# Optimization experiments

Measured on AMD Instinct MI355X. Metric: run time of the kernel, lower is better.

## Reference

```python
import jax, jax.numpy as jnp
import numpy as np
from jax import lax

DT = 0.1
B, T, SD, CD, H = 1024, 200, 64, 32, 512


def setup_inputs() -> dict:
    key = jax.random.key(0)
    k0, k1, k2, k3 = jax.random.split(key, 4)
    scale1 = 1.0 / np.sqrt(SD + CD)
    scale2 = 1.0 / np.sqrt(H)
    return {
        "x0": jax.random.normal(k0, (B, SD), dtype=jnp.float32),
        "controls": jax.random.normal(k1, (B, T, CD), dtype=jnp.float32),
        "W1": jax.random.normal(k2, (SD + CD, H), dtype=jnp.float32) * scale1,
        "b1": jnp.zeros((H,), dtype=jnp.float32),
        "W2": jax.random.normal(k3, (H, SD), dtype=jnp.float32) * scale2,
        "b2": jnp.zeros((SD,), dtype=jnp.float32),
    }


def reference(x0, controls, W1, b1, W2, b2):
    # dynamics: x_{t+1} = x + dt * MLP(concat(x, u)); rollout with true data dependency
    def step(x, u):
        h = jnp.tanh(jnp.concatenate([x, u], axis=-1) @ W1 + b1)  # [B, H]
        x_next = x + DT * (h @ W2 + b2)                           # [B, SD]
        return x_next, x_next

    controls_t = jnp.swapaxes(controls, 0, 1)  # [T, B, CD]
    _, xs = lax.scan(step, x0, controls_t)     # xs: [T, B, SD]
    states = jnp.concatenate([x0[:, None, :], jnp.swapaxes(xs, 0, 1)], axis=1)  # [B, T+1, SD]
    return states
```

## Files before the change

### kernel.cpp

```cpp
#include <hip/hip_runtime.h>
#include <cstddef>


constexpr int B_  = 1024;
constexpr int T_  = 200;
constexpr int SD_ = 64;
constexpr int CD_ = 32;
constexpr int H_  = 512;
constexpr int KD_ = SD_ + CD_;
constexpr float DT_ = 0.1f;
constexpr int ROWS_ = 4;
constexpr int THREADS_ = 1024;
constexpr int KSLICES_ = 4;
constexpr int KLEN_ = KD_ / KSLICES_;
constexpr int CHUNK_ = 32;

typedef float f2 __attribute__((ext_vector_type(2)));

__global__ __launch_bounds__(THREADS_)
void rollout_r12_kernel(
    const float* __restrict__ x0,
    const float* __restrict__ ctrl,
    const float* __restrict__ W1,
    const float* __restrict__ b1,
    const float* __restrict__ W2,
    const float* __restrict__ b2,
    float* __restrict__ out)
{
    __shared__ float xcT[KD_][ROWS_];
    __shared__ float part1[KSLICES_][ROWS_][H_];
    __shared__ float pbuf[ROWS_][H_];
    __shared__ float part2[ROWS_][16][SD_];

    const int tid = threadIdx.x;
    const int r0  = blockIdx.x * ROWS_;

    const int jp    = tid & 255;
    const int ks    = tid >> 8;
    const int j0    = jp * 2;
    const int kbase = ks * KLEN_;
    f2 w1p[KLEN_];
    #pragma unroll
    for (int i = 0; i < KLEN_; ++i)
        w1p[i] = *(const f2*)&W1[(size_t)(kbase + i) * H_ + j0];

    const int wv = tid >> 6;
    const int sl = tid & 63;
    const int jb = wv * CHUNK_;
    float w2p[CHUNK_];
    #pragma unroll
    for (int i = 0; i < CHUNK_; ++i)
        w2p[i] = W2[(size_t)(jb + i) * SD_ + sl];

    const int rF  = tid >> 8;
    const int jjF = (tid & 255) * 2;
    const f2 bj2 = {b1[jjF], b1[jjF + 1]};

    const int rf = (tid >> 6) & 3;
    const int sf = tid & 63;
    const float bs = b2[sf];

    const int  lt = tid - 512;
    const bool loader = (lt >= 0) && (lt < ROWS_ * CD_);
    const int  lr = (lt >> 5) & 3;
    const int  lc = lt & 31;
    const size_t ctrl_base = (size_t)(r0 + lr) * T_ * CD_ + lc;

    if (tid < ROWS_ * SD_) {
        const float v = x0[(size_t)(r0 + rf) * SD_ + sf];
        xcT[sf][rf] = v;
        out[(size_t)(r0 + rf) * (T_ + 1) * SD_ + sf] = v;
    }
    if (loader) xcT[SD_ + lc][lr] = ctrl[ctrl_base];
    __syncthreads();

    for (int t = 0; t < T_; ++t) {
        float cpre = 0.f;
        if (loader && (t + 1 < T_))
            cpre = ctrl[ctrl_base + (size_t)(t + 1) * CD_];

        f2 a0 = {0.f, 0.f}, a1 = {0.f, 0.f}, a2 = {0.f, 0.f}, a3 = {0.f, 0.f};
        #pragma unroll
        for (int i = 0; i < KLEN_; ++i) {
            const float4 xv = *(const float4*)&xcT[kbase + i][0];
            const f2 w = w1p[i];
            a0 = __builtin_elementwise_fma(w, (f2){xv.x, xv.x}, a0);
            a1 = __builtin_elementwise_fma(w, (f2){xv.y, xv.y}, a1);
            a2 = __builtin_elementwise_fma(w, (f2){xv.z, xv.z}, a2);
            a3 = __builtin_elementwise_fma(w, (f2){xv.w, xv.w}, a3);
        }
        *(f2*)&part1[ks][0][j0] = a0;
        *(f2*)&part1[ks][1][j0] = a1;
        *(f2*)&part1[ks][2][j0] = a2;
        *(f2*)&part1[ks][3][j0] = a3;
        __syncthreads();

        {
            f2 s = *(const f2*)&part1[0][rF][jjF];
            s += *(const f2*)&part1[1][rF][jjF];
            s += *(const f2*)&part1[2][rF][jjF];
            s += *(const f2*)&part1[3][rF][jjF];
            s += bj2;
            f2 hv;
            hv.x = tanhf(s.x);
            hv.y = tanhf(s.y);
            *(f2*)&pbuf[rF][jjF] = hv;
            if (loader && (t + 1 < T_))
                xcT[SD_ + lc][lr] = cpre;
        }
        __syncthreads();

        {
            f2 q0 = {0.f, 0.f}, q1 = {0.f, 0.f}, q2 = {0.f, 0.f}, q3 = {0.f, 0.f};
            #pragma unroll
            for (int i4 = 0; i4 < CHUNK_; i4 += 4) {
                const f2 wab = {w2p[i4 + 0], w2p[i4 + 1]};
                const f2 wcd = {w2p[i4 + 2], w2p[i4 + 3]};
                const float4 h0 = *(const float4*)&pbuf[0][jb + i4];
                const float4 h1 = *(const float4*)&pbuf[1][jb + i4];
                const float4 h2 = *(const float4*)&pbuf[2][jb + i4];
                const float4 h3 = *(const float4*)&pbuf[3][jb + i4];
                q0 = __builtin_elementwise_fma((f2){h0.x, h0.y}, wab, q0);
                q0 = __builtin_elementwise_fma((f2){h0.z, h0.w}, wcd, q0);
                q1 = __builtin_elementwise_fma((f2){h1.x, h1.y}, wab, q1);
                q1 = __builtin_elementwise_fma((f2){h1.z, h1.w}, wcd, q1);
                q2 = __builtin_elementwise_fma((f2){h2.x, h2.y}, wab, q2);
                q2 = __builtin_elementwise_fma((f2){h2.z, h2.w}, wcd, q2);
                q3 = __builtin_elementwise_fma((f2){h3.x, h3.y}, wab, q3);
                q3 = __builtin_elementwise_fma((f2){h3.z, h3.w}, wcd, q3);
            }
            part2[0][wv][sl] = q0.x + q0.y;
            part2[1][wv][sl] = q1.x + q1.y;
            part2[2][wv][sl] = q2.x + q2.y;
            part2[3][wv][sl] = q3.x + q3.y;
        }
        __syncthreads();

        if (tid < ROWS_ * SD_) {
            float acc = part2[rf][0][sf];
            #pragma unroll
            for (int c = 1; c < 16; ++c) acc += part2[rf][c][sf];
            const float xnew = xcT[sf][rf] + DT_ * (acc + bs);
            xcT[sf][rf] = xnew;
            out[(size_t)(r0 + rf) * (T_ + 1) * SD_ + (size_t)(t + 1) * SD_ + sf] = xnew;
        }
        __syncthreads();
    }
}

extern "C" void kernel_launch(void* const* d_in, const int* in_sizes, int n_in,
                              void* d_out, int out_size, void* d_ws, size_t ws_size,
                              hipStream_t stream) {
    const float* x0   = (const float*)d_in[0];
    const float* ctrl = (const float*)d_in[1];
    const float* W1   = (const float*)d_in[2];
    const float* b1   = (const float*)d_in[3];
    const float* W2   = (const float*)d_in[4];
    const float* b2   = (const float*)d_in[5];
    float* out = (float*)d_out;

    dim3 grid(B_ / ROWS_);
    dim3 block(THREADS_);
    rollout_r12_kernel<<<grid, block, 0, stream>>>(x0, ctrl, W1, b1, W2, b2, out);
}
```

Before: 707.0 us.

## Reduce layer-1 K-slices with wave shuffles and stage W2 in shared memory

The four K-slices of the first matmul now sit in lanes of the same wavefront, so partial sums are combined with xor-shuffle butterflies instead of going through a shared-memory buffer. This removes one block-wide barrier per timestep. W2 moves from per-thread registers into a 128 KB shared array, which frees registers but adds LDS reads in the second matmul. b1 is also staged in shared memory, and the control-prefetch store moves after the barrier.

```diff
diff --git a/kernel.cpp b/kernel.cpp
--- a/kernel.cpp
+++ b/kernel.cpp
@@ -17,8 +17,17 @@
 
 typedef float f2 __attribute__((ext_vector_type(2)));
 
+__device__ __forceinline__ f2 bfly_ks(f2 v) {
+    f2 r;
+    r.x = __shfl_xor(v.x, 16);  r.y = __shfl_xor(v.y, 16);
+    v.x += r.x;                 v.y += r.y;
+    r.x = __shfl_xor(v.x, 32);  r.y = __shfl_xor(v.y, 32);
+    v.x += r.x;                 v.y += r.y;
+    return v;
+}
+
 __global__ __launch_bounds__(THREADS_)
-void rollout_r12_kernel(
+void rollout_r13_kernel(
     const float* __restrict__ x0,
     const float* __restrict__ ctrl,
     const float* __restrict__ W1,
@@ -27,34 +36,37 @@
     const float* __restrict__ b2,
     float* __restrict__ out)
 {
-    __shared__ float xcT[KD_][ROWS_];
-    __shared__ float part1[KSLICES_][ROWS_][H_];
-    __shared__ float pbuf[ROWS_][H_];
-    __shared__ float part2[ROWS_][16][SD_];
+    __shared__ __align__(16) float w2s[H_][SD_];
+    __shared__ __align__(16) float xcT[KD_][ROWS_];
+    __shared__ __align__(16) float pbuf[ROWS_][H_];
+    __shared__ __align__(16) float part2[ROWS_][16][SD_];
+    __shared__ __align__(16) float b1s[H_];
 
     const int tid = threadIdx.x;
     const int r0  = blockIdx.x * ROWS_;
 
-    const int jp    = tid & 255;
-    const int ks    = tid >> 8;
-    const int j0    = jp * 2;
+    const int lane = tid & 63;
+    const int wvid = tid >> 6;
+    const int ks   = lane >> 4;
+    const int jpl  = lane & 15;
+    const int j0   = (wvid * 16 + jpl) * 2;
     const int kbase = ks * KLEN_;
     f2 w1p[KLEN_];
     #pragma unroll
     for (int i = 0; i < KLEN_; ++i)
         w1p[i] = *(const f2*)&W1[(size_t)(kbase + i) * H_ + j0];
 
-    const int wv = tid >> 6;
-    const int sl = tid & 63;
-    const int jb = wv * CHUNK_;
-    float w2p[CHUNK_];
-    #pragma unroll
-    for (int i = 0; i < CHUNK_; ++i)
-        w2p[i] = W2[(size_t)(jb + i) * SD_ + sl];
+    {
+        const float4* __restrict__ src = (const float4*)W2;
+        float4* dst = (float4*)&w2s[0][0];
+        #pragma unroll
+        for (int i = 0; i < 8; ++i)
+            dst[i * THREADS_ + tid] = src[i * THREADS_ + tid];
+    }
+    if (tid < H_) b1s[tid] = b1[tid];
 
-    const int rF  = tid >> 8;
-    const int jjF = (tid & 255) * 2;
-    const f2 bj2 = {b1[jjF], b1[jjF + 1]};
+    const int sl = lane;
+    const int jb = wvid * CHUNK_;
 
     const int rf = (tid >> 6) & 3;
     const int sf = tid & 63;
@@ -89,33 +101,34 @@
             a2 = __builtin_elementwise_fma(w, (f2){xv.z, xv.z}, a2);
             a3 = __builtin_elementwise_fma(w, (f2){xv.w, xv.w}, a3);
         }
-        *(f2*)&part1[ks][0][j0] = a0;
-        *(f2*)&part1[ks][1][j0] = a1;
-        *(f2*)&part1[ks][2][j0] = a2;
-        *(f2*)&part1[ks][3][j0] = a3;
-        __syncthreads();
-
+        a0 = bfly_ks(a0);  a1 = bfly_ks(a1);
+        a2 = bfly_ks(a2);  a3 = bfly_ks(a3);
         {
-            f2 s = *(const f2*)&part1[0][rF][jjF];
-            s += *(const f2*)&part1[1][rF][jjF];
-            s += *(const f2*)&part1[2][rF][jjF];
-            s += *(const f2*)&part1[3][rF][jjF];
-            s += bj2;
+            const bool kb0 = (ks & 1) != 0;
+            const bool kb1 = (ks & 2) != 0;
+            const f2 s01 = kb0 ? a1 : a0;
+            const f2 s23 = kb0 ? a3 : a2;
+            const f2 sel = kb1 ? s23 : s01;
+            const f2 bj  = *(const f2*)&b1s[j0];
             f2 hv;
-            hv.x = tanhf(s.x);
-            hv.y = tanhf(s.y);
-            *(f2*)&pbuf[rF][jjF] = hv;
-            if (loader && (t + 1 < T_))
-                xcT[SD_ + lc][lr] = cpre;
+            hv.x = tanhf(sel.x + bj.x);
+            hv.y = tanhf(sel.y + bj.y);
+            *(f2*)&pbuf[ks][j0] = hv;
         }
         __syncthreads();
 
+        if (loader && (t + 1 < T_))
+            xcT[SD_ + lc][lr] = cpre;
         {
             f2 q0 = {0.f, 0.f}, q1 = {0.f, 0.f}, q2 = {0.f, 0.f}, q3 = {0.f, 0.f};
             #pragma unroll
             for (int i4 = 0; i4 < CHUNK_; i4 += 4) {
-                const f2 wab = {w2p[i4 + 0], w2p[i4 + 1]};
-                const f2 wcd = {w2p[i4 + 2], w2p[i4 + 3]};
+                const float wa = w2s[jb + i4 + 0][sl];
+                const float wb = w2s[jb + i4 + 1][sl];
+                const float wc = w2s[jb + i4 + 2][sl];
+                const float wd = w2s[jb + i4 + 3][sl];
+                const f2 wab = {wa, wb};
+                const f2 wcd = {wc, wd};
                 const float4 h0 = *(const float4*)&pbuf[0][jb + i4];
                 const float4 h1 = *(const float4*)&pbuf[1][jb + i4];
                 const float4 h2 = *(const float4*)&pbuf[2][jb + i4];
@@ -129,10 +142,10 @@
                 q3 = __builtin_elementwise_fma((f2){h3.x, h3.y}, wab, q3);
                 q3 = __builtin_elementwise_fma((f2){h3.z, h3.w}, wcd, q3);
             }
-            part2[0][wv][sl] = q0.x + q0.y;
-            part2[1][wv][sl] = q1.x + q1.y;
-            part2[2][wv][sl] = q2.x + q2.y;
-            part2[3][wv][sl] = q3.x + q3.y;
+            part2[0][wvid][sl] = q0.x + q0.y;
+            part2[1][wvid][sl] = q1.x + q1.y;
+            part2[2][wvid][sl] = q2.x + q2.y;
+            part2[3][wvid][sl] = q3.x + q3.y;
         }
         __syncthreads();
 
@@ -161,5 +174,5 @@
 
     dim3 grid(B_ / ROWS_);
     dim3 block(THREADS_);
-    rollout_r12_kernel<<<grid, block, 0, stream>>>(x0, ctrl, W1, b1, W2, b2, out);
+    rollout_r13_kernel<<<grid, block, 0, stream>>>(x0, ctrl, W1, b1, W2, b2, out);
 }
```

Result: slower. 827.8 us (+17.1%).

## Repartition both matmuls across threads with more K slices and paired outputs

Applied to the files above, without the earlier changes.

The first matmul moves from 4 to 8 K slices, and each thread now computes two column pairs 256 apart, so each LDS load of the shared input feeds twice as many FMAs. The second matmul switches to f2 outputs over paired state dims with 16-row h chunks, which doubles the number of partial sums to 32. The final reductions become trees to shorten dependency chains. The trade-off is more part1 and part2 LDS traffic and reduction work in exchange for fewer input loads per FMA, with unchanged register footprint.

```diff
diff --git a/kernel.cpp b/kernel.cpp
--- a/kernel.cpp
+++ b/kernel.cpp
@@ -11,14 +11,13 @@
 constexpr float DT_ = 0.1f;
 constexpr int ROWS_ = 4;
 constexpr int THREADS_ = 1024;
-constexpr int KSLICES_ = 4;
+constexpr int KSLICES_ = 8;
 constexpr int KLEN_ = KD_ / KSLICES_;
-constexpr int CHUNK_ = 32;
 
 typedef float f2 __attribute__((ext_vector_type(2)));
 
 __global__ __launch_bounds__(THREADS_)
-void rollout_r12_kernel(
+void rollout_r15_kernel(
     const float* __restrict__ x0,
     const float* __restrict__ ctrl,
     const float* __restrict__ W1,
@@ -27,30 +26,35 @@
     const float* __restrict__ b2,
     float* __restrict__ out)
 {
-    __shared__ float xcT[KD_][ROWS_];
-    __shared__ float part1[KSLICES_][ROWS_][H_];
-    __shared__ float pbuf[ROWS_][H_];
-    __shared__ float part2[ROWS_][16][SD_];
+    __shared__ __align__(16) float xcT[KD_][ROWS_];
+    __shared__ __align__(16) float part1[KSLICES_][ROWS_][H_];
+    __shared__ __align__(16) float pbuf[ROWS_][H_];
+    __shared__ __align__(16) float part2[ROWS_][32][SD_];
 
     const int tid = threadIdx.x;
     const int r0  = blockIdx.x * ROWS_;
 
-    const int jp    = tid & 255;
-    const int ks    = tid >> 8;
-    const int j0    = jp * 2;
+    const int jpg   = tid & 127;
+    const int ks    = tid >> 7;
+    const int j0    = jpg * 2;
     const int kbase = ks * KLEN_;
-    f2 w1p[KLEN_];
+    f2 w1a[KLEN_], w1b[KLEN_];
     #pragma unroll
-    for (int i = 0; i < KLEN_; ++i)
-        w1p[i] = *(const f2*)&W1[(size_t)(kbase + i) * H_ + j0];
+    for (int i = 0; i < KLEN_; ++i) {
+        w1a[i] = *(const f2*)&W1[(size_t)(kbase + i) * H_ + j0];
+        w1b[i] = *(const f2*)&W1[(size_t)(kbase + i) * H_ + j0 + 256];
+    }
 
-    const int wv = tid >> 6;
-    const int sl = tid & 63;
-    const int jb = wv * CHUNK_;
-    float w2p[CHUNK_];
+    const int wv    = tid >> 6;
+    const int lane  = tid & 63;
+    const int l5    = lane >> 5;
+    const int sfp   = lane & 31;
+    const int sf0   = sfp * 2;
+    const int hbase = wv * 32 + l5 * 16;
+    f2 w2p[16];
     #pragma unroll
-    for (int i = 0; i < CHUNK_; ++i)
-        w2p[i] = W2[(size_t)(jb + i) * SD_ + sl];
+    for (int i = 0; i < 16; ++i)
+        w2p[i] = *(const f2*)&W2[(size_t)(hbase + i) * SD_ + sf0];
 
     const int rF  = tid >> 8;
     const int jjF = (tid & 255) * 2;
@@ -79,28 +83,38 @@
         if (loader && (t + 1 < T_))
             cpre = ctrl[ctrl_base + (size_t)(t + 1) * CD_];
 
-        f2 a0 = {0.f, 0.f}, a1 = {0.f, 0.f}, a2 = {0.f, 0.f}, a3 = {0.f, 0.f};
+        f2 a0 = {0.f,0.f}, a1 = {0.f,0.f}, a2 = {0.f,0.f}, a3 = {0.f,0.f};
+        f2 b0 = {0.f,0.f}, b1v = {0.f,0.f}, b2v = {0.f,0.f}, b3 = {0.f,0.f};
         #pragma unroll
         for (int i = 0; i < KLEN_; ++i) {
             const float4 xv = *(const float4*)&xcT[kbase + i][0];
-            const f2 w = w1p[i];
-            a0 = __builtin_elementwise_fma(w, (f2){xv.x, xv.x}, a0);
-            a1 = __builtin_elementwise_fma(w, (f2){xv.y, xv.y}, a1);
-            a2 = __builtin_elementwise_fma(w, (f2){xv.z, xv.z}, a2);
-            a3 = __builtin_elementwise_fma(w, (f2){xv.w, xv.w}, a3);
+            const f2 wa = w1a[i];
+            const f2 wb = w1b[i];
+            a0  = __builtin_elementwise_fma(wa, (f2){xv.x, xv.x}, a0);
+            a1  = __builtin_elementwise_fma(wa, (f2){xv.y, xv.y}, a1);
+            a2  = __builtin_elementwise_fma(wa, (f2){xv.z, xv.z}, a2);
+            a3  = __builtin_elementwise_fma(wa, (f2){xv.w, xv.w}, a3);
+            b0  = __builtin_elementwise_fma(wb, (f2){xv.x, xv.x}, b0);
+            b1v = __builtin_elementwise_fma(wb, (f2){xv.y, xv.y}, b1v);
+            b2v = __builtin_elementwise_fma(wb, (f2){xv.z, xv.z}, b2v);
+            b3  = __builtin_elementwise_fma(wb, (f2){xv.w, xv.w}, b3);
         }
         *(f2*)&part1[ks][0][j0] = a0;
         *(f2*)&part1[ks][1][j0] = a1;
         *(f2*)&part1[ks][2][j0] = a2;
         *(f2*)&part1[ks][3][j0] = a3;
+        *(f2*)&part1[ks][0][j0 + 256] = b0;
+        *(f2*)&part1[ks][1][j0 + 256] = b1v;
+        *(f2*)&part1[ks][2][j0 + 256] = b2v;
+        *(f2*)&part1[ks][3][j0 + 256] = b3;
         __syncthreads();
 
         {
-            f2 s = *(const f2*)&part1[0][rF][jjF];
-            s += *(const f2*)&part1[1][rF][jjF];
-            s += *(const f2*)&part1[2][rF][jjF];
-            s += *(const f2*)&part1[3][rF][jjF];
-            s += bj2;
+            const f2 s0 = *(const f2*)&part1[0][rF][jjF] + *(const f2*)&part1[1][rF][jjF];
+            const f2 s1 = *(const f2*)&part1[2][rF][jjF] + *(const f2*)&part1[3][rF][jjF];
+            const f2 s2 = *(const f2*)&part1[4][rF][jjF] + *(const f2*)&part1[5][rF][jjF];
+            const f2 s3 = *(const f2*)&part1[6][rF][jjF] + *(const f2*)&part1[7][rF][jjF];
+            const f2 s  = ((s0 + s1) + (s2 + s3)) + bj2;
             f2 hv;
             hv.x = tanhf(s.x);
             hv.y = tanhf(s.y);
@@ -111,35 +125,48 @@
         __syncthreads();
 
         {
-            f2 q0 = {0.f, 0.f}, q1 = {0.f, 0.f}, q2 = {0.f, 0.f}, q3 = {0.f, 0.f};
+            f2 q0 = {0.f,0.f}, q1 = {0.f,0.f}, q2 = {0.f,0.f}, q3 = {0.f,0.f};
             #pragma unroll
-            for (int i4 = 0; i4 < CHUNK_; i4 += 4) {
-                const f2 wab = {w2p[i4 + 0], w2p[i4 + 1]};
-                const f2 wcd = {w2p[i4 + 2], w2p[i4 + 3]};
-                const float4 h0 = *(const float4*)&pbuf[0][jb + i4];
-                const float4 h1 = *(const float4*)&pbuf[1][jb + i4];
-                const float4 h2 = *(const float4*)&pbuf[2][jb + i4];
-                const float4 h3 = *(const float4*)&pbuf[3][jb + i4];
-                q0 = __builtin_elementwise_fma((f2){h0.x, h0.y}, wab, q0);
-                q0 = __builtin_elementwise_fma((f2){h0.z, h0.w}, wcd, q0);
-                q1 = __builtin_elementwise_fma((f2){h1.x, h1.y}, wab, q1);
-                q1 = __builtin_elementwise_fma((f2){h1.z, h1.w}, wcd, q1);
-                q2 = __builtin_elementwise_fma((f2){h2.x, h2.y}, wab, q2);
-                q2 = __builtin_elementwise_fma((f2){h2.z, h2.w}, wcd, q2);
-                q3 = __builtin_elementwise_fma((f2){h3.x, h3.y}, wab, q3);
-                q3 = __builtin_elementwise_fma((f2){h3.z, h3.w}, wcd, q3);
+            for (int i4 = 0; i4 < 16; i4 += 4) {
+                const float4 h0 = *(const float4*)&pbuf[0][hbase + i4];
+                const float4 h1 = *(const float4*)&pbuf[1][hbase + i4];
+                const float4 h2 = *(const float4*)&pbuf[2][hbase + i4];
+                const float4 h3 = *(const float4*)&pbuf[3][hbase + i4];
+                q0 = __builtin_elementwise_fma((f2){h0.x, h0.x}, w2p[i4 + 0], q0);
+                q0 = __builtin_elementwise_fma((f2){h0.y, h0.y}, w2p[i4 + 1], q0);
+                q0 = __builtin_elementwise_fma((f2){h0.z, h0.z}, w2p[i4 + 2], q0);
+                q0 = __builtin_elementwise_fma((f2){h0.w, h0.w}, w2p[i4 + 3], q0);
+                q1 = __builtin_elementwise_fma((f2){h1.x, h1.x}, w2p[i4 + 0], q1);
+                q1 = __builtin_elementwise_fma((f2){h1.y, h1.y}, w2p[i4 + 1], q1);
+                q1 = __builtin_elementwise_fma((f2){h1.z, h1.z}, w2p[i4 + 2], q1);
+                q1 = __builtin_elementwise_fma((f2){h1.w, h1.w}, w2p[i4 + 3], q1);
+                q2 = __builtin_elementwise_fma((f2){h2.x, h2.x}, w2p[i4 + 0], q2);
+                q2 = __builtin_elementwise_fma((f2){h2.y, h2.y}, w2p[i4 + 1], q2);
+                q2 = __builtin_elementwise_fma((f2){h2.z, h2.z}, w2p[i4 + 2], q2);
+                q2 = __builtin_elementwise_fma((f2){h2.w, h2.w}, w2p[i4 + 3], q2);
+                q3 = __builtin_elementwise_fma((f2){h3.x, h3.x}, w2p[i4 + 0], q3);
+                q3 = __builtin_elementwise_fma((f2){h3.y, h3.y}, w2p[i4 + 1], q3);
+                q3 = __builtin_elementwise_fma((f2){h3.z, h3.z}, w2p[i4 + 2], q3);
+                q3 = __builtin_elementwise_fma((f2){h3.w, h3.w}, w2p[i4 + 3], q3);
             }
-            part2[0][wv][sl] = q0.x + q0.y;
-            part2[1][wv][sl] = q1.x + q1.y;
-            part2[2][wv][sl] = q2.x + q2.y;
-            part2[3][wv][sl] = q3.x + q3.y;
+            const int c = wv * 2 + l5;
+            *(f2*)&part2[0][c][sf0] = q0;
+            *(f2*)&part2[1][c][sf0] = q1;
+            *(f2*)&part2[2][c][sf0] = q2;
+            *(f2*)&part2[3][c][sf0] = q3;
         }
         __syncthreads();
 
         if (tid < ROWS_ * SD_) {
-            float acc = part2[rf][0][sf];
+            float v[32];
             #pragma unroll
-            for (int c = 1; c < 16; ++c) acc += part2[rf][c][sf];
+            for (int c = 0; c < 32; ++c) v[c] = part2[rf][c][sf];
+            float s[8];
+            #pragma unroll
+            for (int c = 0; c < 8; ++c)
+                s[c] = (v[4*c] + v[4*c+1]) + (v[4*c+2] + v[4*c+3]);
+            const float acc = ((s[0] + s[1]) + (s[2] + s[3]))
+                            + ((s[4] + s[5]) + (s[6] + s[7]));
             const float xnew = xcT[sf][rf] + DT_ * (acc + bs);
             xcT[sf][rf] = xnew;
             out[(size_t)(r0 + rf) * (T_ + 1) * SD_ + (size_t)(t + 1) * SD_ + sf] = xnew;
@@ -161,5 +188,5 @@
 
     dim3 grid(B_ / ROWS_);
     dim3 block(THREADS_);
-    rollout_r12_kernel<<<grid, block, 0, stream>>>(x0, ctrl, W1, b1, W2, b2, out);
+    rollout_r15_kernel<<<grid, block, 0, stream>>>(x0, ctrl, W1, b1, W2, b2, out);
 }
```

Result: faster. 664.2 us (-6.0%).
